# Kernel tuning notes

Measured on AMD Instinct MI355X. Metric: run time of the kernel, lower is better.

## Reference

```python
import jax, jax.numpy as jnp
import numpy as np

N = 50000   # nodes
E = 600000  # edges (avg degree 12)
D = 128     # feature dim (input_dim == output_dim for residual)
G = 8       # graphs in batch
EPS = 1e-5


def setup_inputs() -> dict:
    key = jax.random.key(0)
    ks = jax.random.split(key, 8)
    x = jax.random.normal(ks[0], (N, D), dtype=jnp.float32)
    edge_index = jax.random.randint(ks[1], (2, E), 0, N)
    batch = jnp.sort(jax.random.randint(ks[2], (N,), 0, G))
    s = 1.0 / np.sqrt(D)
    Wl = jax.random.normal(ks[3], (D, D), dtype=jnp.float32) * s
    bl = jax.random.normal(ks[4], (D,), dtype=jnp.float32) * s
    Wr = jax.random.normal(ks[5], (D, D), dtype=jnp.float32) * s
    return {
        "x": x,
        "edge_index": edge_index,
        "batch": batch,
        "num_graphs": G,
        "Wl": Wl,
        "bl": bl,
        "Wr": Wr,
        "gn_weight": jnp.ones((D,), jnp.float32),
        "gn_bias": jnp.zeros((D,), jnp.float32),
        "mean_scale": jnp.ones((D,), jnp.float32),
    }


def reference(x, edge_index, batch, num_graphs, Wl, bl, Wr, gn_weight, gn_bias, mean_scale):
    n = x.shape[0]
    src, dst = edge_index[0], edge_index[1]

    # SAGEConv: mean-aggregate neighbor (source) features at target nodes
    ones_e = jnp.ones(src.shape[0], dtype=x.dtype)
    deg = jax.ops.segment_sum(ones_e, dst, num_segments=n)          # [N]
    agg = jax.ops.segment_sum(x[src], dst, num_segments=n)          # [N, D]
    agg = agg / jnp.maximum(deg, 1.0)[:, None]
    f = agg @ Wl.T + bl + x @ Wr.T                                  # lin_l(agg) + lin_r(x)

    # exact (erf) GELU, as torch F.gelu default
    f = jax.nn.gelu(f, approximate=False)

    # GraphNorm: per-graph statistics with learnable mean_scale
    ones_n = jnp.ones(n, dtype=x.dtype)
    cnt = jax.ops.segment_sum(ones_n, batch, num_segments=num_graphs)[:, None]  # [G,1]
    mean = jax.ops.segment_sum(f, batch, num_segments=num_graphs) / cnt         # [G,D]
    out = f - mean_scale * mean[batch]
    var = jax.ops.segment_sum(out * out, batch, num_segments=num_graphs) / cnt  # [G,D]
    out = out / jnp.sqrt(var[batch] + EPS) * gn_weight + gn_bias

    # dropout is identity in eval mode; residual add
    return out + x
```

## Files before the change

kernel.cpp:

```cpp
#include <hip/hip_runtime.h>

#define D 128
#define NGRAPH 8
#define EPS 1e-5f
#define BINCAP 512

typedef __attribute__((ext_vector_type(4))) float f32x4;
typedef __attribute__((ext_vector_type(2))) float f32x2;
typedef __attribute__((ext_vector_type(8))) short s16x8;

__device__ __forceinline__ unsigned short f2bf(float f) {
    unsigned int u = __float_as_uint(f);
    u += 0x7fffu + ((u >> 16) & 1u);
    return (unsigned short)(u >> 16);
}
__device__ __forceinline__ float blo(unsigned int u) { return __uint_as_float(u << 16); }
__device__ __forceinline__ float bhi(unsigned int u) { return __uint_as_float(u & 0xffff0000u); }

__global__ __launch_bounds__(256) void prep_fill_kernel(
    const float* __restrict__ Wl, const float* __restrict__ Wr,
    unsigned short* __restrict__ Bsw,
    const float* __restrict__ x, unsigned int* __restrict__ xb,
    unsigned int* __restrict__ xf8,
    const int* __restrict__ batch, int* __restrict__ bnd,
    const int* __restrict__ ei, unsigned int* __restrict__ bcnt,
    unsigned int* __restrict__ bbuf,
    int N, int E, int Npad, int fillB)
{
    int b = blockIdx.x;
    if (b < 128) {
        int t = b * 256 + threadIdx.x;
        int j    = t & 7;
        int ln   = (t >> 3) & 63;
        int ks   = (t >> 9) & 7;
        int tile = t >> 12;
        int k = ks * 32 + (ln >> 4) * 8 + j;
        int d = tile * 16 + (ln & 15);
        float v = (k < 128) ? Wl[(size_t)d * 128 + k] : Wr[(size_t)d * 128 + (k - 128)];
        Bsw[t] = f2bf(v);
    } else if (b == 128) {
        int g = threadIdx.x;
        if (g <= NGRAPH) {
            int lo = 0, hi = N;
            while (lo < hi) {
                int mid = (lo + hi) >> 1;
                if (batch[mid] < g) lo = mid + 1; else hi = mid;
            }
            bnd[g] = lo;
        }
    } else if (b < 129 + fillB) {
        int e = (b - 129) * 256 + threadIdx.x;
        if (e < E) {
            int dst = ei[E + e];
            int src = ei[e];
            int bin = dst >> 5;
            unsigned int pos = atomicAdd(&bcnt[(size_t)bin * 16], 1u);
            if (pos < BINCAP)
                bbuf[(size_t)bin * BINCAP + pos] =
                    (unsigned int)src | ((unsigned int)(dst & 31) << 16);
        }
    } else {
        int iu = (b - 129 - fillB) * 256 + threadIdx.x;
        if (iu < Npad * 32) {
            int n = iu >> 5, slot = iu & 31;
            if (iu < N * 32) {
                float4 p = *(const float4*)(x + (size_t)iu * 4);
                uint2 o;
                o.x = (unsigned int)f2bf(p.x) | ((unsigned int)f2bf(p.y) << 16);
                o.y = (unsigned int)f2bf(p.z) | ((unsigned int)f2bf(p.w) << 16);
                *(uint2*)(xb + (size_t)iu * 2) = o;
                int u8 = __builtin_amdgcn_cvt_pk_fp8_f32(p.x, p.y, 0, false);
                u8     = __builtin_amdgcn_cvt_pk_fp8_f32(p.z, p.w, u8, true);
                xf8[(size_t)n * 32 + slot] = (unsigned int)u8;
            } else {
                *(uint2*)(xb + (size_t)iu * 2) = make_uint2(0u, 0u);
                xf8[(size_t)n * 32 + slot] = 0u;
            }
        }
    }
}

__global__ __launch_bounds__(256, 8) void fused_kernel(
    const unsigned short* __restrict__ xf8,
    const unsigned int* __restrict__ bcnt, const unsigned int* __restrict__ bbuf,
    const unsigned short* __restrict__ xb16, const unsigned short* __restrict__ Bsw,
    const float* __restrict__ bl, const int* __restrict__ batch,
    float* __restrict__ gsum, float* __restrict__ gsumsq,
    unsigned short* __restrict__ fout16, int N)
{
    __shared__ unsigned int aggL[32][68];
    __shared__ unsigned short sortedL[BINCAP];
    __shared__ int histL[32];
    __shared__ int startL[32];
    __shared__ int offsL[32];

    int wave = threadIdx.x >> 6, lane = threadIdx.x & 63;
    int bin = blockIdx.x;
    int nblk0 = bin * 32;

    if (threadIdx.x < 32) histL[threadIdx.x] = 0;
    __syncthreads();

    int ec = (int)bcnt[(size_t)bin * 16];
    if (ec > BINCAP) ec = BINCAP;
    const unsigned int* bb = bbuf + (size_t)bin * BINCAP;
    int t0 = threadIdx.x, t1 = threadIdx.x + 256;
    unsigned int ent0 = 0u, ent1 = 0u;
    if (t0 < ec) { ent0 = bb[t0]; atomicAdd(&histL[ent0 >> 16], 1); }
    if (t1 < ec) { ent1 = bb[t1]; atomicAdd(&histL[ent1 >> 16], 1); }
    __syncthreads();
    if (threadIdx.x == 0) {
        int acc = 0;
        for (int i = 0; i < 32; ++i) { startL[i] = acc; offsL[i] = acc; acc += histL[i]; }
    }
    __syncthreads();
    if (t0 < ec) { int p = atomicAdd(&offsL[ent0 >> 16], 1); sortedL[p] = (unsigned short)(ent0 & 0xffffu); }
    if (t1 < ec) { int p = atomicAdd(&offsL[ent1 >> 16], 1); sortedL[p] = (unsigned short)(ent1 & 0xffffu); }
    __syncthreads();

#pragma unroll
    for (int s = 0; s < 8; ++s) {
        int ln = wave * 8 + s;
        int dgn = histL[ln];
        int base = startL[ln];
        float a0 = 0.0f, a1 = 0.0f;
        int i = 0;
        for (; i + 8 <= dgn; i += 8) {
            int nb[8];
#pragma unroll
            for (int k = 0; k < 8; ++k) nb[k] = sortedL[base + i + k];
            unsigned short u[8];
#pragma unroll
            for (int k = 0; k < 8; ++k) u[k] = xf8[(size_t)nb[k] * 64 + lane];
#pragma unroll
            for (int k = 0; k < 8; ++k) {
                f32x2 d2 = __builtin_amdgcn_cvt_pk_f32_fp8((int)(unsigned int)u[k], false);
                a0 += d2[0]; a1 += d2[1];
            }
        }
        for (; i < dgn; ++i) {
            int nb = sortedL[base + i];
            f32x2 d2 = __builtin_amdgcn_cvt_pk_f32_fp8(
                (int)(unsigned int)xf8[(size_t)nb * 64 + lane], false);
            a0 += d2[0]; a1 += d2[1];
        }
        float iv = 1.0f / (float)(dgn > 0 ? dgn : 1);
        aggL[ln][lane] =
            (unsigned int)f2bf(a0 * iv) | ((unsigned int)f2bf(a1 * iv) << 16);
    }
    __syncthreads();

    int row0 = nblk0 + (wave >> 1) * 16;
    int th = wave & 1;
    int m = lane & 15, quad = lane >> 4;
    int r = row0 + m;
    int lr = (wave >> 1) * 16 + m;

    s16x8 afrag[8];
#pragma unroll
    for (int ks = 0; ks < 4; ++ks)
        afrag[ks] = *(const s16x8*)&aggL[lr][ks * 16 + quad * 4];
    const unsigned short* xp = xb16 + (size_t)r * 128 + quad * 8;
#pragma unroll
    for (int ks = 0; ks < 4; ++ks) afrag[4 + ks] = *(const s16x8*)(xp + ks * 32);

    int nbase = row0;
    bool uni = (nbase + 15 < N) && (batch[nbase] == batch[nbase + 15]);
    int gu = (nbase < N) ? batch[nbase] : 0;

#pragma unroll
    for (int t = 0; t < 4; ++t) {
        int tile = th * 4 + t;
        f32x4 acc = {0.0f, 0.0f, 0.0f, 0.0f};
        const s16x8* bptr = (const s16x8*)Bsw + (size_t)(tile * 8) * 64 + lane;
#pragma unroll
        for (int ks = 0; ks < 8; ++ks)
            acc = __builtin_amdgcn_mfma_f32_16x16x32_bf16(afrag[ks], bptr[(size_t)ks * 64], acc, 0, 0, 0);
        int d = tile * 16 + m;
        float bias = bl[d];
        float sm = 0.0f, sq = 0.0f;
#pragma unroll
        for (int rr = 0; rr < 4; ++rr) {
            int node = nbase + quad * 4 + rr;
            float v = acc[rr] + bias;
            float g = 0.5f * v * (1.0f + erff(v * 0.70710678118654752f));
            if (node < N) {
                fout16[(size_t)node * 128 + d] = f2bf(g);
                if (uni) { sm += g; sq += g * g; }
                else {
                    int gg = batch[node];
                    unsafeAtomicAdd(&gsum[gg * D + d], g);
                    unsafeAtomicAdd(&gsumsq[gg * D + d], g * g);
                }
            }
        }
        if (uni) {
            sm += __shfl_xor(sm, 16, 64); sm += __shfl_xor(sm, 32, 64);
            sq += __shfl_xor(sq, 16, 64); sq += __shfl_xor(sq, 32, 64);
            if (quad == 0) {
                unsafeAtomicAdd(&gsum[gu * D + d], sm);
                unsafeAtomicAdd(&gsumsq[gu * D + d], sq);
            }
        }
    }
}

__global__ __launch_bounds__(256) void final_kernel(
    const unsigned int* __restrict__ f16, const float* __restrict__ x,
    const int* __restrict__ batch, const int* __restrict__ bnd,
    const float* __restrict__ gsum, const float* __restrict__ gsumsq,
    const float* __restrict__ ms,
    const float* __restrict__ gw, const float* __restrict__ gb,
    float* __restrict__ out, int N)
{
    int t = blockIdx.x * 256 + threadIdx.x;
    if (t >= N * (D / 4)) return;
    int n  = t >> 5;
    int d0 = (t & 31) * 4;
    int g  = batch[n];
    int c  = bnd[g + 1] - bnd[g];
    float invc = 1.0f / (float)(c > 0 ? c : 1);
    size_t row = (size_t)n * D + d0;
    uint2 fu = *(const uint2*)(f16 + (size_t)n * 64 + (d0 >> 1));
    float4 fv = make_float4(blo(fu.x), bhi(fu.x), blo(fu.y), bhi(fu.y));
    float4 xv = *(const float4*)(x + row);
    float4 s1 = *(const float4*)(gsum + g * D + d0);
    float4 s2 = *(const float4*)(gsumsq + g * D + d0);
    float4 msv = *(const float4*)(ms + d0);
    float4 gwv = *(const float4*)(gw + d0);
    float4 gbv = *(const float4*)(gb + d0);
    float4 o;
    {
        float mu = s1.x * invc, q = s2.x * invc, a = msv.x * mu;
        float sc = rsqrtf(q - 2.0f * a * mu + a * a + EPS);
        o.x = (fv.x - a) * sc * gwv.x + gbv.x + xv.x;
    }
    {
        float mu = s1.y * invc, q = s2.y * invc, a = msv.y * mu;
        float sc = rsqrtf(q - 2.0f * a * mu + a * a + EPS);
        o.y = (fv.y - a) * sc * gwv.y + gbv.y + xv.y;
    }
    {
        float mu = s1.z * invc, q = s2.z * invc, a = msv.z * mu;
        float sc = rsqrtf(q - 2.0f * a * mu + a * a + EPS);
        o.z = (fv.z - a) * sc * gwv.z + gbv.z + xv.z;
    }
    {
        float mu = s1.w * invc, q = s2.w * invc, a = msv.w * mu;
        float sc = rsqrtf(q - 2.0f * a * mu + a * a + EPS);
        o.w = (fv.w - a) * sc * gwv.w + gbv.w + xv.w;
    }
    *(float4*)(out + row) = o;
}

extern "C" void kernel_launch(void* const* d_in, const int* in_sizes, int n_in,
                              void* d_out, int out_size, void* d_ws, size_t ws_size,
                              hipStream_t stream)
{
    const float* x     = (const float*)d_in[0];
    const int*   ei    = (const int*)d_in[1];
    const int*   batch = (const int*)d_in[2];
    const float* Wl = (const float*)d_in[4];
    const float* bl = (const float*)d_in[5];
    const float* Wr = (const float*)d_in[6];
    const float* gw = (const float*)d_in[7];
    const float* gb = (const float*)d_in[8];
    const float* ms = (const float*)d_in[9];
    float* out = (float*)d_out;

    int N = in_sizes[0] / D;
    int E = in_sizes[1] / 2;
    int NBLK = (N + 63) / 64;
    int Npad = NBLK * 64;
    int NB32 = Npad / 32;

    unsigned int*   fout16 = (unsigned int*)d_ws;
    unsigned int*   xf8  = fout16 + (size_t)Npad * 64;
    unsigned int*   xb   = xf8 + (size_t)Npad * 32;
    unsigned short* Bsw  = (unsigned short*)(xb + (size_t)Npad * 64);
    float* gsum   = (float*)(Bsw + 32768);
    float* gsumsq = gsum + NGRAPH * D;
    unsigned int* pad  = (unsigned int*)(gsumsq + NGRAPH * D);
    unsigned int* bcnt = pad + 4;
    int*          bnd  = (int*)(bcnt + (size_t)NB32 * 16);
    unsigned int* bbuf = (unsigned int*)(bnd + (NGRAPH + 1));

    hipMemsetAsync(gsum, 0,
                   (2 * NGRAPH * D) * sizeof(float) + 4 * sizeof(unsigned int)
                   + (size_t)NB32 * 16 * sizeof(unsigned int), stream);

    int fillB = (E + 255) / 256;
    int xbB   = (Npad * 32 + 255) / 256;
    prep_fill_kernel<<<129 + fillB + xbB, 256, 0, stream>>>(
        Wl, Wr, Bsw, x, xb, xf8, batch, bnd, ei, bcnt, bbuf, N, E, Npad, fillB);

    fused_kernel<<<NB32, 256, 0, stream>>>(
        (const unsigned short*)xf8, bcnt, bbuf,
        (const unsigned short*)xb, Bsw, bl, batch,
        gsum, gsumsq, (unsigned short*)fout16, N);

    {
        int threads = N * (D / 4);
        final_kernel<<<(threads + 255) / 256, 256, 0, stream>>>(
            fout16, x, batch, bnd, gsum, gsumsq, ms, gw, gb, out, N);
    }
}
```

Before: 180.1 us.

## Shrink fused-kernel block to 16 nodes with 8-node edge bins

Edges are binned per 8 destination nodes instead of 32, and each fused block now handles 16 nodes (two bins), with each wave covering 4 nodes in the aggregation and 2 output tiles in the MFMA stage. This roughly doubles the number of blocks, giving more parallelism and latency hiding on the gather, and lowers shared memory per block. In exchange the per-bin capacity is cut to 160 entries (average is about 96 per bin), so a high-degree bin could overflow and drop edges. There are also more global atomics on bin counters and smaller per-block work.

```diff
diff --git a/kernel.cpp b/kernel.cpp
--- a/kernel.cpp
+++ b/kernel.cpp
@@ -3,7 +3,7 @@
 #define D 128
 #define NGRAPH 8
 #define EPS 1e-5f
-#define BINCAP 512
+#define BINCAP 160
 
 typedef __attribute__((ext_vector_type(4))) float f32x4;
 typedef __attribute__((ext_vector_type(2))) float f32x2;
@@ -53,11 +53,11 @@
         if (e < E) {
             int dst = ei[E + e];
             int src = ei[e];
-            int bin = dst >> 5;
+            int bin = dst >> 3;
             unsigned int pos = atomicAdd(&bcnt[(size_t)bin * 16], 1u);
             if (pos < BINCAP)
                 bbuf[(size_t)bin * BINCAP + pos] =
-                    (unsigned int)src | ((unsigned int)(dst & 31) << 16);
+                    (unsigned int)src | ((unsigned int)(dst & 7) << 16);
         }
     } else {
         int iu = (b - 129 - fillB) * 256 + threadIdx.x;
@@ -88,39 +88,50 @@
     float* __restrict__ gsum, float* __restrict__ gsumsq,
     unsigned short* __restrict__ fout16, int N)
 {
-    __shared__ unsigned int aggL[32][68];
-    __shared__ unsigned short sortedL[BINCAP];
-    __shared__ int histL[32];
-    __shared__ int startL[32];
-    __shared__ int offsL[32];
+    __shared__ unsigned int aggL[16][68];
+    __shared__ unsigned short sortedL[2 * BINCAP];
+    __shared__ int histL[16];
+    __shared__ int startL[16];
+    __shared__ int offsL[16];
 
     int wave = threadIdx.x >> 6, lane = threadIdx.x & 63;
-    int bin = blockIdx.x;
-    int nblk0 = bin * 32;
-
-    if (threadIdx.x < 32) histL[threadIdx.x] = 0;
-    __syncthreads();
-
-    int ec = (int)bcnt[(size_t)bin * 16];
-    if (ec > BINCAP) ec = BINCAP;
-    const unsigned int* bb = bbuf + (size_t)bin * BINCAP;
+    int nblk0 = blockIdx.x * 16;
+    int bin0 = blockIdx.x * 2;
+
+    if (threadIdx.x < 16) histL[threadIdx.x] = 0;
+    __syncthreads();
+
+    int ec0 = (int)bcnt[(size_t)bin0 * 16];       if (ec0 > BINCAP) ec0 = BINCAP;
+    int ec1 = (int)bcnt[(size_t)(bin0 + 1) * 16]; if (ec1 > BINCAP) ec1 = BINCAP;
+    int ec = ec0 + ec1;
+    const unsigned int* bb0 = bbuf + (size_t)bin0 * BINCAP;
+    const unsigned int* bb1 = bbuf + (size_t)(bin0 + 1) * BINCAP;
     int t0 = threadIdx.x, t1 = threadIdx.x + 256;
     unsigned int ent0 = 0u, ent1 = 0u;
-    if (t0 < ec) { ent0 = bb[t0]; atomicAdd(&histL[ent0 >> 16], 1); }
-    if (t1 < ec) { ent1 = bb[t1]; atomicAdd(&histL[ent1 >> 16], 1); }
+    int dl0 = 0, dl1 = 0;
+    if (t0 < ec) {
+        ent0 = (t0 < ec0) ? bb0[t0] : bb1[t0 - ec0];
+        dl0  = (int)(ent0 >> 16) + ((t0 < ec0) ? 0 : 8);
+        atomicAdd(&histL[dl0], 1);
+    }
+    if (t1 < ec) {
+        ent1 = (t1 < ec0) ? bb0[t1] : bb1[t1 - ec0];
+        dl1  = (int)(ent1 >> 16) + ((t1 < ec0) ? 0 : 8);
+        atomicAdd(&histL[dl1], 1);
+    }
     __syncthreads();
     if (threadIdx.x == 0) {
         int acc = 0;
-        for (int i = 0; i < 32; ++i) { startL[i] = acc; offsL[i] = acc; acc += histL[i]; }
-    }
-    __syncthreads();
-    if (t0 < ec) { int p = atomicAdd(&offsL[ent0 >> 16], 1); sortedL[p] = (unsigned short)(ent0 & 0xffffu); }
-    if (t1 < ec) { int p = atomicAdd(&offsL[ent1 >> 16], 1); sortedL[p] = (unsigned short)(ent1 & 0xffffu); }
-    __syncthreads();
-
-#pragma unroll
-    for (int s = 0; s < 8; ++s) {
-        int ln = wave * 8 + s;
+        for (int i = 0; i < 16; ++i) { startL[i] = acc; offsL[i] = acc; acc += histL[i]; }
+    }
+    __syncthreads();
+    if (t0 < ec) { int p = atomicAdd(&offsL[dl0], 1); sortedL[p] = (unsigned short)(ent0 & 0xffffu); }
+    if (t1 < ec) { int p = atomicAdd(&offsL[dl1], 1); sortedL[p] = (unsigned short)(ent1 & 0xffffu); }
+    __syncthreads();
+
+#pragma unroll
+    for (int s = 0; s < 4; ++s) {
+        int ln = wave * 4 + s;
         int dgn = histL[ln];
         int base = startL[ln];
         float a0 = 0.0f, a1 = 0.0f;
@@ -150,27 +161,24 @@
     }
     __syncthreads();
 
-    int row0 = nblk0 + (wave >> 1) * 16;
-    int th = wave & 1;
     int m = lane & 15, quad = lane >> 4;
-    int r = row0 + m;
-    int lr = (wave >> 1) * 16 + m;
+    int r = nblk0 + m;
 
     s16x8 afrag[8];
 #pragma unroll
     for (int ks = 0; ks < 4; ++ks)
-        afrag[ks] = *(const s16x8*)&aggL[lr][ks * 16 + quad * 4];
+        afrag[ks] = *(const s16x8*)&aggL[m][ks * 16 + quad * 4];
     const unsigned short* xp = xb16 + (size_t)r * 128 + quad * 8;
 #pragma unroll
     for (int ks = 0; ks < 4; ++ks) afrag[4 + ks] = *(const s16x8*)(xp + ks * 32);
 
-    int nbase = row0;
+    int nbase = nblk0;
     bool uni = (nbase + 15 < N) && (batch[nbase] == batch[nbase + 15]);
     int gu = (nbase < N) ? batch[nbase] : 0;
 
 #pragma unroll
-    for (int t = 0; t < 4; ++t) {
-        int tile = th * 4 + t;
+    for (int t = 0; t < 2; ++t) {
+        int tile = wave * 2 + t;
         f32x4 acc = {0.0f, 0.0f, 0.0f, 0.0f};
         const s16x8* bptr = (const s16x8*)Bsw + (size_t)(tile * 8) * 64 + lane;
 #pragma unroll
@@ -272,7 +280,8 @@
     int E = in_sizes[1] / 2;
     int NBLK = (N + 63) / 64;
     int Npad = NBLK * 64;
-    int NB32 = Npad / 32;
+    int NBIN = Npad / 8;
+    int NB16 = Npad / 16;
 
     unsigned int*   fout16 = (unsigned int*)d_ws;
     unsigned int*   xf8  = fout16 + (size_t)Npad * 64;
@@ -282,19 +291,19 @@
     float* gsumsq = gsum + NGRAPH * D;
     unsigned int* pad  = (unsigned int*)(gsumsq + NGRAPH * D);
     unsigned int* bcnt = pad + 4;
-    int*          bnd  = (int*)(bcnt + (size_t)NB32 * 16);
+    int*          bnd  = (int*)(bcnt + (size_t)NBIN * 16);
     unsigned int* bbuf = (unsigned int*)(bnd + (NGRAPH + 1));
 
     hipMemsetAsync(gsum, 0,
                    (2 * NGRAPH * D) * sizeof(float) + 4 * sizeof(unsigned int)
-                   + (size_t)NB32 * 16 * sizeof(unsigned int), stream);
+                   + (size_t)NBIN * 16 * sizeof(unsigned int), stream);
 
     int fillB = (E + 255) / 256;
     int xbB   = (Npad * 32 + 255) / 256;
     prep_fill_kernel<<<129 + fillB + xbB, 256, 0, stream>>>(
         Wl, Wr, Bsw, x, xb, xf8, batch, bnd, ei, bcnt, bbuf, N, E, Npad, fillB);
 
-    fused_kernel<<<NB32, 256, 0, stream>>>(
+    fused_kernel<<<NB16, 256, 0, stream>>>(
         (const unsigned short*)xf8, bcnt, bbuf,
         (const unsigned short*)xb, Bsw, bl, batch,
         gsum, gsumsq, (unsigned short*)fout16, N);
```

After: 183.0 us. Within noise of the previous version (+1.6%).
